# Optimization experiments

Measured on AMD Instinct MI355X. Metric: run time of the kernel, lower is better.

The kernel has to match this reference:

```python
import jax, jax.numpy as jnp
import numpy as np

B, S, D, H, A = 64, 1024, 64, 512, 16


def setup_inputs() -> dict:
    key = jax.random.key(0)
    ks = jax.random.split(key, 13)
    s = 0.02
    return {
        "x": jax.random.normal(ks[0], (B, S, D), jnp.float32),
        "W_ih": jax.random.normal(ks[1], (3 * H, 2 * D), jnp.float32) * s,
        "W_hh": jax.random.normal(ks[2], (3 * H, H), jnp.float32) * s,
        "b_ih": jax.random.normal(ks[3], (3 * H,), jnp.float32) * s,
        "b_hh": jax.random.normal(ks[4], (3 * H,), jnp.float32) * s,
        "fc_w": jax.random.normal(ks[5], (H, H), jnp.float32) * s,
        "fc_b": jax.random.normal(ks[6], (H,), jnp.float32) * s,
        "out_w": jax.random.normal(ks[7], (A, H), jnp.float32) * s,
        "out_b": jax.random.normal(ks[8], (A,), jnp.float32) * s,
        "cb_w1": jax.random.normal(ks[9], (H, H), jnp.float32) * s,
        "cb_b1": jax.random.normal(ks[10], (H,), jnp.float32) * s,
        "cb_w2": jax.random.normal(ks[11], (D, H), jnp.float32) * s,
        "cb_b2": jax.random.normal(ks[12], (D,), jnp.float32) * s,
    }


def _gru_cell(inp, h, W_ih, W_hh, b_ih, b_hh):
    # PyTorch GRU cell: gates ordered (reset, update, new)
    gi = inp @ W_ih.T + b_ih            # [B, 3H]
    gh = h @ W_hh.T + b_hh              # [B, 3H]
    ir, iz, inn = jnp.split(gi, 3, axis=-1)
    hr, hz, hn = jnp.split(gh, 3, axis=-1)
    r = jax.nn.sigmoid(ir + hr)
    z = jax.nn.sigmoid(iz + hz)
    n = jnp.tanh(inn + r * hn)
    return (1.0 - z) * n + z * h


def reference(x, W_ih, W_hh, b_ih, b_hh, fc_w, fc_b, out_w, out_b, cb_w1, cb_b1, cb_w2, cb_b2):
    b = x.shape[0]
    h0 = jnp.zeros((b, H), x.dtype)
    pred0 = jnp.zeros((b, D), x.dtype)

    def step(carry, x_t):
        h, pred = carry
        inp = jnp.concatenate([x_t, pred], axis=-1)        # [B, 2D]
        h_new = _gru_cell(inp, h, W_ih, W_hh, b_ih, b_hh)  # [B, H]
        pred_new = jax.nn.relu(h_new @ cb_w1.T + cb_b1) @ cb_w2.T + cb_b2  # [B, D]
        return (h_new, pred_new), (h_new, pred_new)

    (h_last, _), (outs, preds) = jax.lax.scan(step, (h0, pred0), jnp.swapaxes(x, 0, 1))
    out = jnp.swapaxes(outs, 0, 1)       # [B, S, H]  (gru_out == hidden for 1-layer GRU)
    cb_preds = jnp.swapaxes(preds, 0, 1) # [B, S, D]
    ca1_out = jax.nn.relu(out @ fc_w.T + fc_b)
    q = ca1_out @ out_w.T + out_b        # [B, S, A]
    hidden = h_last[None]                # [1, B, H] like torch GRU hidden
    return q, cb_preds, hidden, ca1_out
```

## Files before the change

### kernel.cpp

```cpp
#include <hip/hip_runtime.h>
#include <hip/hip_fp16.h>


#define B_ 64
#define S_ 1024
#define D_ 64
#define H_ 512
#define A_ 16

#define WG_CHUNKS 240
#define WG_U4     (8 * WG_CHUNKS * 64)
#define WU_U4     (8 * 64 * 64)

union V16 {
    uint4   u;
    float4  f;
    __half2 h[4];
};

__device__ __forceinline__ void dot_block(const uint4* __restrict__ wp, int off,
                                          const V16* __restrict__ a, float& acc) {
    V16 w0, w1, w2, w3;
    w0.u = wp[off];
    w1.u = wp[off + 64];
    w2.u = wp[off + 128];
    w3.u = wp[off + 192];
    __half2 p = __hmul2(w0.h[0], a[0].h[0]);
    __half2 q = __hmul2(w0.h[1], a[0].h[1]);
    p = __hfma2(w0.h[2], a[0].h[2], p);
    q = __hfma2(w0.h[3], a[0].h[3], q);
    p = __hfma2(w1.h[0], a[1].h[0], p);
    q = __hfma2(w1.h[1], a[1].h[1], q);
    p = __hfma2(w1.h[2], a[1].h[2], p);
    q = __hfma2(w1.h[3], a[1].h[3], q);
    p = __hfma2(w2.h[0], a[2].h[0], p);
    q = __hfma2(w2.h[1], a[2].h[1], q);
    p = __hfma2(w2.h[2], a[2].h[2], p);
    q = __hfma2(w2.h[3], a[2].h[3], q);
    p = __hfma2(w3.h[0], a[3].h[0], p);
    q = __hfma2(w3.h[1], a[3].h[1], q);
    p = __hfma2(w3.h[2], a[3].h[2], p);
    q = __hfma2(w3.h[3], a[3].h[3], q);
    float2 fp = __half22float2(p), fq = __half22float2(q);
    acc += (fp.x + fp.y) + (fq.x + fq.y);
}

__global__ __launch_bounds__(256) void k_convert(
    const float* __restrict__ W_ih,
    const float* __restrict__ W_hh,
    const float* __restrict__ cb_w1,
    uint4* __restrict__ wg, uint4* __restrict__ wu)
{
    int idx = blockIdx.x * 256 + threadIdx.x;
    if (idx < WG_U4) {
        int blk  = idx / (WG_CHUNKS * 64);
        int rem  = idx % (WG_CHUNKS * 64);
        int c    = rem / 64, lane = rem % 64;
        int j    = blk * 64 + lane;
        const float* src;
        if (c < 48) {
            int kb = c / 12, r = c % 12, g = r >> 2, q = r & 3;
            src = W_ih + (size_t)(g * 512 + j) * 128 + kb * 32 + q * 8;
        } else {
            int c2 = c - 48;
            int kb = c2 / 12, r = c2 % 12, g = r >> 2, q = r & 3;
            src = W_hh + (size_t)(g * 512 + j) * 512 + kb * 32 + q * 8;
        }
        V16 o;
#pragma unroll
        for (int i = 0; i < 4; ++i) o.h[i] = __floats2half2_rn(src[2 * i], src[2 * i + 1]);
        wg[idx] = o.u;
    } else if (idx < WG_U4 + WU_U4) {
        int i2   = idx - WG_U4;
        int blk  = i2 / 4096;
        int rem  = i2 % 4096;
        int c    = rem / 64, lane = rem % 64;
        int j    = blk * 64 + lane;
        int kb   = c >> 2, q = c & 3;
        const float* src = cb_w1 + (size_t)j * 512 + kb * 32 + q * 8;
        V16 o;
#pragma unroll
        for (int i = 0; i < 4; ++i) o.h[i] = __floats2half2_rn(src[2 * i], src[2 * i + 1]);
        wu[i2] = o.u;
    }
}

__global__ __launch_bounds__(512) void k_recur(
    const float* __restrict__ x,
    const uint4* __restrict__ wg,
    const uint4* __restrict__ wu,
    const float* __restrict__ b_ih,
    const float* __restrict__ b_hh,
    const float* __restrict__ cb_b1,
    const float* __restrict__ cb_b2,
    const float* __restrict__ cb_w2,
    float* __restrict__ hist,
    float* __restrict__ hidden,
    float* __restrict__ cbp)
{
    __shared__ __align__(16) __half2 s_h2[256];
    __shared__ __align__(16) __half2 s_inp2[64];
    __shared__ __align__(16) float   s_u[512];

    const int tid = threadIdx.x;
    const int b   = blockIdx.x;
    const int j   = tid;

    const float bihr = b_ih[j], bihz = b_ih[512 + j], bihn = b_ih[1024 + j];
    const float bhhr = b_hh[j], bhhz = b_hh[512 + j], bhhn = b_hh[1024 + j];
    const float b1j  = cb_b1[j];
    const int   pd   = tid >> 3, psl = tid & 7;
    const float b2d  = cb_b2[pd];
    const float* pw  = cb_w2 + (size_t)pd * 512 + psl * 64;

    float hprev = 0.f;
    if (tid < 256) s_h2[tid] = __floats2half2_rn(0.f, 0.f);
    if (tid < 32) {
        float2 xv = *(const float2*)(x + ((size_t)b * S_) * D_ + tid * 2);
        s_inp2[tid] = __floats2half2_rn(xv.x, xv.y);
    } else if (tid < 64) {
        s_inp2[tid] = __floats2half2_rn(0.f, 0.f);
    }
    __syncthreads();

    const uint4* wgb = wg + (size_t)(tid >> 6) * (WG_CHUNKS * 64) + (tid & 63);
    const uint4* wub = wu + (size_t)(tid >> 6) * (64 * 64) + (tid & 63);

    for (int t = 0; t < S_; ++t) {
        const uint4* wp = wgb;
        float accr = 0.f, accz = 0.f, accni = 0.f, accnh = 0.f;
        V16 a[4];
#pragma unroll
        for (int kb = 0; kb < 4; ++kb) {
            const float4* ap = (const float4*)s_inp2;
            a[0].f = ap[kb * 4 + 0]; a[1].f = ap[kb * 4 + 1];
            a[2].f = ap[kb * 4 + 2]; a[3].f = ap[kb * 4 + 3];
            dot_block(wp,   0, a, accr);
            dot_block(wp, 256, a, accz);
            dot_block(wp, 512, a, accni);
            wp += 12 * 64;
        }
#pragma unroll 2
        for (int kb = 0; kb < 16; ++kb) {
            const float4* ap = (const float4*)s_h2;
            a[0].f = ap[kb * 4 + 0]; a[1].f = ap[kb * 4 + 1];
            a[2].f = ap[kb * 4 + 2]; a[3].f = ap[kb * 4 + 3];
            dot_block(wp,   0, a, accr);
            dot_block(wp, 256, a, accz);
            dot_block(wp, 512, a, accnh);
            wp += 12 * 64;
        }
        float r = 1.f / (1.f + __expf(-(accr + bihr + bhhr)));
        float z = 1.f / (1.f + __expf(-(accz + bihz + bhhz)));
        float n = tanhf(accni + bihn + r * (accnh + bhhn));
        float hnew = (1.f - z) * n + z * hprev;
        __syncthreads();

        float oth = __shfl_xor(hnew, 1);
        if (!(tid & 1)) s_h2[tid >> 1] = __floats2half2_rn(hnew, oth);
        hist[((size_t)b * S_ + t) * H_ + j] = hnew;
        if (t == S_ - 1) hidden[(size_t)b * H_ + j] = hnew;
        hprev = hnew;
        __syncthreads();

        if (tid < 32 && t + 1 < S_) {
            float2 xv = *(const float2*)(x + ((size_t)b * S_ + (t + 1)) * D_ + tid * 2);
            s_inp2[tid] = __floats2half2_rn(xv.x, xv.y);
        }
        const uint4* wp2 = wub;
        float accu = 0.f;
#pragma unroll 2
        for (int kb = 0; kb < 16; ++kb) {
            const float4* ap = (const float4*)s_h2;
            a[0].f = ap[kb * 4 + 0]; a[1].f = ap[kb * 4 + 1];
            a[2].f = ap[kb * 4 + 2]; a[3].f = ap[kb * 4 + 3];
            dot_block(wp2, 0, a, accu);
            wp2 += 256;
        }
        s_u[tid] = fmaxf(accu + b1j, 0.f);
        __syncthreads();

        float pa = 0.f;
        const float4* uv = (const float4*)(s_u + psl * 64);
#pragma unroll
        for (int i = 0; i < 16; ++i) {
            float4 uu = uv[i];
            float4 ww = ((const float4*)pw)[i];
            pa += uu.x * ww.x + uu.y * ww.y + uu.z * ww.z + uu.w * ww.w;
        }
        pa += __shfl_xor(pa, 1);
        pa += __shfl_xor(pa, 2);
        pa += __shfl_xor(pa, 4);
        float pv = pa + b2d;
        if (psl == 0) cbp[((size_t)b * S_ + t) * 64 + pd] = pv;
        float po = __shfl_xor(pv, 8);
        if (psl == 0 && !(pd & 1)) s_inp2[32 + (pd >> 1)] = __floats2half2_rn(pv, po);
        __syncthreads();
    }
}

__global__ __launch_bounds__(256) void k_fc_inplace(
    float* __restrict__ hist,
    const float* __restrict__ fc_w,
    const float* __restrict__ fc_b)
{
    __shared__ __align__(16) float s_a[16 * 516];
    const int tid = threadIdx.x;
    const int r = tid & 15;
    const int jset = tid >> 4;
    const int row0 = blockIdx.x * 16;

    for (int i = tid; i < 2048; i += 256) {
        int rr = i >> 7, f = i & 127;
        float4 v = *(const float4*)(hist + (size_t)(row0 + rr) * H_ + f * 4);
        *(float4*)(s_a + rr * 516 + f * 4) = v;
    }
    __syncthreads();

    float acc[32];
#pragma unroll
    for (int jj = 0; jj < 32; ++jj) acc[jj] = 0.f;

    const float4* arow = (const float4*)(s_a + r * 516);
    for (int k4 = 0; k4 < 128; ++k4) {
        float4 a = arow[k4];
#pragma unroll
        for (int jj = 0; jj < 32; ++jj) {
            int j = jset + (jj << 4);
            float4 w = *(const float4*)(fc_w + (size_t)j * 512 + k4 * 4);
            acc[jj] += a.x * w.x + a.y * w.y + a.z * w.z + a.w * w.w;
        }
    }

    float* crow = hist + (size_t)(row0 + r) * H_;
#pragma unroll
    for (int jj = 0; jj < 32; ++jj) {
        int j = jset + (jj << 4);
        float v = acc[jj] + fc_b[j];
        crow[j] = fmaxf(v, 0.f);
    }
}

__global__ __launch_bounds__(256) void k_q(
    const float* __restrict__ ca1,
    const float* __restrict__ out_w,
    const float* __restrict__ out_b,
    float* __restrict__ q)
{
    __shared__ __align__(16) float s_a[16 * 516];
    __shared__ __align__(16) float s_w[16 * 516];
    const int tid = threadIdx.x;
    const int r = tid >> 4;
    const int a_ = tid & 15;
    const int row0 = blockIdx.x * 16;

    for (int i = tid; i < 2048; i += 256) {
        int rr = i >> 7, f = i & 127;
        float4 v = *(const float4*)(ca1 + (size_t)(row0 + rr) * H_ + f * 4);
        *(float4*)(s_a + rr * 516 + f * 4) = v;
    }
    for (int i = tid; i < 2048; i += 256) {
        int rr = i >> 7, f = i & 127;
        float4 v = *(const float4*)(out_w + (size_t)rr * 512 + f * 4);
        *(float4*)(s_w + rr * 516 + f * 4) = v;
    }
    __syncthreads();

    const float4* arow = (const float4*)(s_a + r * 516);
    const float4* wrow = (const float4*)(s_w + a_ * 516);
    float acc = 0.f;
#pragma unroll 8
    for (int k4 = 0; k4 < 128; ++k4) {
        float4 a = arow[k4];
        float4 w = wrow[k4];
        acc += a.x * w.x + a.y * w.y + a.z * w.z + a.w * w.w;
    }
    q[(size_t)(row0 + r) * A_ + a_] = acc + out_b[a_];
}

extern "C" void kernel_launch(void* const* d_in, const int* in_sizes, int n_in,
                              void* d_out, int out_size, void* d_ws, size_t ws_size,
                              hipStream_t stream) {
    const float* x     = (const float*)d_in[0];
    const float* W_ih  = (const float*)d_in[1];
    const float* W_hh  = (const float*)d_in[2];
    const float* b_ih  = (const float*)d_in[3];
    const float* b_hh  = (const float*)d_in[4];
    const float* fc_w  = (const float*)d_in[5];
    const float* fc_b  = (const float*)d_in[6];
    const float* out_w = (const float*)d_in[7];
    const float* out_b = (const float*)d_in[8];
    const float* cb_w1 = (const float*)d_in[9];
    const float* cb_b1 = (const float*)d_in[10];
    const float* cb_w2 = (const float*)d_in[11];
    const float* cb_b2 = (const float*)d_in[12];

    float* q_out  = (float*)d_out;
    float* cbp    = q_out + (size_t)B_ * S_ * A_;
    float* hidden = cbp + (size_t)B_ * S_ * D_;
    float* ca1    = hidden + (size_t)B_ * H_;

    uint4* wg = (uint4*)d_ws;
    uint4* wu = wg + WG_U4;

    k_convert<<<(WG_U4 + WU_U4) / 256, 256, 0, stream>>>(W_ih, W_hh, cb_w1, wg, wu);
    k_recur<<<B_, 512, 0, stream>>>(x, wg, wu, b_ih, b_hh, cb_b1, cb_b2, cb_w2,
                                    ca1, hidden, cbp);
    k_fc_inplace<<<4096, 256, 0, stream>>>(ca1, fc_w, fc_b);
    k_q<<<4096, 256, 0, stream>>>(ca1, out_w, out_b, q_out);
}
```

Measured before the change: 37.48 ms.

## Split GRU recurrence across 128 persistent workgroups with global barriers

Replaces the per-batch recurrence (64 workgroups, each streaming all weights every step) with 128 persistent workgroups that each own 4 hidden units across all batches, so each workgroup keeps a small weight slice and reuses it over 64 batch rows. Hidden state, the ReLU intermediate and predictions move through global memory and are synchronised by custom flag-based grid barriers, three per timestep. This is meant to cut the per-step weight traffic from global memory and spread work over more compute units, at the cost of three device-wide barriers per step and a deadlock risk if the workgroups are not all co-resident, which a timeout flag guards against.

```diff
diff --git a/kernel.cpp b/kernel.cpp
--- a/kernel.cpp
+++ b/kernel.cpp
@@ -8,9 +8,16 @@
 #define H_ 512
 #define A_ 16
 
-#define WG_CHUNKS 240
-#define WG_U4     (8 * WG_CHUNKS * 64)
-#define WU_U4     (8 * 64 * 64)
+#define OFF_WGX   0
+#define OFF_WGI   98304
+#define OFF_WUX   122880
+#define OFF_SYNC  155648
+#define OFF_H2    156192
+#define OFF_U2    164384
+#define OFF_PRED2 172576
+#define WS_TOTAL  173088
+
+#define NWG 128
 
 union V16 {
     uint4   u;
@@ -18,184 +25,283 @@
     __half2 h[4];
 };
 
-__device__ __forceinline__ void dot_block(const uint4* __restrict__ wp, int off,
-                                          const V16* __restrict__ a, float& acc) {
-    V16 w0, w1, w2, w3;
-    w0.u = wp[off];
-    w1.u = wp[off + 64];
-    w2.u = wp[off + 128];
-    w3.u = wp[off + 192];
-    __half2 p = __hmul2(w0.h[0], a[0].h[0]);
-    __half2 q = __hmul2(w0.h[1], a[0].h[1]);
-    p = __hfma2(w0.h[2], a[0].h[2], p);
-    q = __hfma2(w0.h[3], a[0].h[3], q);
-    p = __hfma2(w1.h[0], a[1].h[0], p);
-    q = __hfma2(w1.h[1], a[1].h[1], q);
-    p = __hfma2(w1.h[2], a[1].h[2], p);
-    q = __hfma2(w1.h[3], a[1].h[3], q);
-    p = __hfma2(w2.h[0], a[2].h[0], p);
-    q = __hfma2(w2.h[1], a[2].h[1], q);
-    p = __hfma2(w2.h[2], a[2].h[2], p);
-    q = __hfma2(w2.h[3], a[2].h[3], q);
-    p = __hfma2(w3.h[0], a[3].h[0], p);
-    q = __hfma2(w3.h[1], a[3].h[1], q);
-    p = __hfma2(w3.h[2], a[3].h[2], p);
-    q = __hfma2(w3.h[3], a[3].h[3], q);
-    float2 fp = __half22float2(p), fq = __half22float2(q);
-    acc += (fp.x + fp.y) + (fq.x + fq.y);
-}
-
 __global__ __launch_bounds__(256) void k_convert(
     const float* __restrict__ W_ih,
     const float* __restrict__ W_hh,
     const float* __restrict__ cb_w1,
-    uint4* __restrict__ wg, uint4* __restrict__ wu)
+    uint4* __restrict__ ws)
 {
     int idx = blockIdx.x * 256 + threadIdx.x;
-    if (idx < WG_U4) {
-        int blk  = idx / (WG_CHUNKS * 64);
-        int rem  = idx % (WG_CHUNKS * 64);
-        int c    = rem / 64, lane = rem % 64;
-        int j    = blk * 64 + lane;
-        const float* src;
-        if (c < 48) {
-            int kb = c / 12, r = c % 12, g = r >> 2, q = r & 3;
-            src = W_ih + (size_t)(g * 512 + j) * 128 + kb * 32 + q * 8;
-        } else {
-            int c2 = c - 48;
-            int kb = c2 / 12, r = c2 % 12, g = r >> 2, q = r & 3;
-            src = W_hh + (size_t)(g * 512 + j) * 512 + kb * 32 + q * 8;
-        }
-        V16 o;
-#pragma unroll
-        for (int i = 0; i < 4; ++i) o.h[i] = __floats2half2_rn(src[2 * i], src[2 * i + 1]);
-        wg[idx] = o.u;
-    } else if (idx < WG_U4 + WU_U4) {
-        int i2   = idx - WG_U4;
-        int blk  = i2 / 4096;
-        int rem  = i2 % 4096;
-        int c    = rem / 64, lane = rem % 64;
-        int j    = blk * 64 + lane;
-        int kb   = c >> 2, q = c & 3;
-        const float* src = cb_w1 + (size_t)j * 512 + kb * 32 + q * 8;
-        V16 o;
-#pragma unroll
-        for (int i = 0; i < 4; ++i) o.h[i] = __floats2half2_rn(src[2 * i], src[2 * i + 1]);
-        wu[i2] = o.u;
-    }
-}
-
-__global__ __launch_bounds__(512) void k_recur(
+    const float* src;
+    if (idx < OFF_WGI) {
+        int wg = idx / 768, rem = idx % 768;
+        int r = rem >> 6, c = (rem >> 4) & 3, q = rem & 15;
+        int g = r >> 2, jj = r & 3;
+        src = W_hh + (size_t)(g * 512 + wg * 4 + jj) * 512 + c * 128 + q * 8;
+    } else if (idx < OFF_WUX) {
+        int i2 = idx - OFF_WGI;
+        int wg = i2 / 192, rem = i2 % 192;
+        int r = rem >> 4, c = (rem >> 2) & 3, q2 = rem & 3;
+        int g = r >> 2, jj = r & 3;
+        src = W_ih + (size_t)(g * 512 + wg * 4 + jj) * 128 + c * 32 + q2 * 8;
+    } else if (idx < OFF_SYNC) {
+        int i2 = idx - OFF_WUX;
+        int wg = i2 / 256, rem = i2 % 256;
+        int jr = rem >> 6, c = (rem >> 4) & 3, q = rem & 15;
+        src = cb_w1 + (size_t)(wg * 4 + jr) * 512 + c * 128 + q * 8;
+    } else if (idx < WS_TOTAL) {
+        ws[idx] = make_uint4(0u, 0u, 0u, 0u);
+        return;
+    } else return;
+    V16 o;
+#pragma unroll
+    for (int i = 0; i < 4; ++i) o.h[i] = __floats2half2_rn(src[2 * i], src[2 * i + 1]);
+    ws[idx] = o.u;
+}
+
+__device__ __forceinline__ int poll_ge(unsigned* p, unsigned bn, unsigned* dead) {
+    unsigned it = 0;
+    while (__hip_atomic_load(p, __ATOMIC_RELAXED, __HIP_MEMORY_SCOPE_AGENT) < bn) {
+        __builtin_amdgcn_s_sleep(2);
+        if ((++it & 1023u) == 0u) {
+            if (__hip_atomic_load(dead, __ATOMIC_RELAXED, __HIP_MEMORY_SCOPE_AGENT) != 0u) return 1;
+            if (it > (1u << 24)) {
+                __hip_atomic_store(dead, 1u, __ATOMIC_RELAXED, __HIP_MEMORY_SCOPE_AGENT);
+                return 1;
+            }
+        }
+    }
+    return 0;
+}
+
+__device__ __forceinline__ int gbar(unsigned* flags, unsigned* dead, unsigned bn,
+                                    unsigned* s_flag) {
+    const int tid = threadIdx.x;
+    __syncthreads();
+    if (tid == 0) *s_flag = 0u;
+    __syncthreads();
+    if (tid == 0) {
+        __builtin_amdgcn_fence(__ATOMIC_RELEASE, "agent");
+        __hip_atomic_store(flags + blockIdx.x * 16, bn, __ATOMIC_RELAXED,
+                           __HIP_MEMORY_SCOPE_AGENT);
+    }
+    if (tid < NWG) {
+        if (poll_ge(flags + tid * 16, bn, dead)) *s_flag = 1u;
+    }
+    __syncthreads();
+    if (tid == 0) __builtin_amdgcn_fence(__ATOMIC_ACQUIRE, "agent");
+    __syncthreads();
+    return *s_flag != 0u;
+}
+
+__global__ __launch_bounds__(256) void k_recur(
+    const uint4* __restrict__ wsb,
+    unsigned* __restrict__ syncw,
+    uint4* __restrict__ h2u4,
+    float* __restrict__ u2f,
+    uint4* __restrict__ pred2u4,
     const float* __restrict__ x,
-    const uint4* __restrict__ wg,
-    const uint4* __restrict__ wu,
-    const float* __restrict__ b_ih,
-    const float* __restrict__ b_hh,
-    const float* __restrict__ cb_b1,
-    const float* __restrict__ cb_b2,
+    const float* __restrict__ b_ih, const float* __restrict__ b_hh,
+    const float* __restrict__ cb_b1, const float* __restrict__ cb_b2,
     const float* __restrict__ cb_w2,
     float* __restrict__ hist,
     float* __restrict__ hidden,
     float* __restrict__ cbp)
 {
-    __shared__ __align__(16) __half2 s_h2[256];
-    __shared__ __align__(16) __half2 s_inp2[64];
-    __shared__ __align__(16) float   s_u[512];
-
+    __shared__ unsigned s_flag;
     const int tid = threadIdx.x;
-    const int b   = blockIdx.x;
-    const int j   = tid;
-
-    const float bihr = b_ih[j], bihz = b_ih[512 + j], bihn = b_ih[1024 + j];
-    const float bhhr = b_hh[j], bhhz = b_hh[512 + j], bhhn = b_hh[1024 + j];
-    const float b1j  = cb_b1[j];
-    const int   pd   = tid >> 3, psl = tid & 7;
-    const float b2d  = cb_b2[pd];
-    const float* pw  = cb_w2 + (size_t)pd * 512 + psl * 64;
-
-    float hprev = 0.f;
-    if (tid < 256) s_h2[tid] = __floats2half2_rn(0.f, 0.f);
-    if (tid < 32) {
-        float2 xv = *(const float2*)(x + ((size_t)b * S_) * D_ + tid * 2);
-        s_inp2[tid] = __floats2half2_rn(xv.x, xv.y);
-    } else if (tid < 64) {
-        s_inp2[tid] = __floats2half2_rn(0.f, 0.f);
-    }
-    __syncthreads();
-
-    const uint4* wgb = wg + (size_t)(tid >> 6) * (WG_CHUNKS * 64) + (tid & 63);
-    const uint4* wub = wu + (size_t)(tid >> 6) * (64 * 64) + (tid & 63);
+    const int wg = blockIdx.x;
+    const int b = tid >> 2;
+    const int c = tid & 3;
+    const int j4 = wg * 4;
+
+    unsigned* dead = syncw + 2048;
+
+    const uint4* wgxP = wsb + OFF_WGX + wg * 768 + c * 16;
+    const uint4* wgiP = wsb + OFF_WGI + wg * 192 + c * 4;
+    const uint4* wuxP = wsb + OFF_WUX + wg * 256 + c * 16;
+
+    float bias_r[4], bias_z[4], bias_ni[4], bias_nh[4], bias_u[4];
+#pragma unroll
+    for (int jj = 0; jj < 4; ++jj) {
+        int j = j4 + jj;
+        bias_r[jj]  = b_ih[j] + b_hh[j];
+        bias_z[jj]  = b_ih[512 + j] + b_hh[512 + j];
+        bias_ni[jj] = b_ih[1024 + j];
+        bias_nh[jj] = b_hh[1024 + j];
+        bias_u[jj]  = cb_b1[j];
+    }
+    const int dl = tid >> 3, oct = tid & 7;
+    const int pb = wg >> 1, d = (wg & 1) * 32 + dl;
+    const float bias_p = cb_b2[d];
+
+    float hprev[4] = {0.f, 0.f, 0.f, 0.f};
+
+    const uint4* hrow0 = h2u4 + b * 64 + c * 16;
+    const uint4* hrow1 = h2u4 + 4096 + b * 64 + c * 16;
+    uint2* h2w0 = (uint2*)h2u4 + b * 128 + wg;
+    uint2* h2w1 = ((uint2*)(h2u4 + 4096)) + b * 128 + wg;
+    __half* pred2h = (__half*)pred2u4;
+
+    unsigned bn = 0;
 
     for (int t = 0; t < S_; ++t) {
-        const uint4* wp = wgb;
-        float accr = 0.f, accz = 0.f, accni = 0.f, accnh = 0.f;
-        V16 a[4];
-#pragma unroll
-        for (int kb = 0; kb < 4; ++kb) {
-            const float4* ap = (const float4*)s_inp2;
-            a[0].f = ap[kb * 4 + 0]; a[1].f = ap[kb * 4 + 1];
-            a[2].f = ap[kb * 4 + 2]; a[3].f = ap[kb * 4 + 3];
-            dot_block(wp,   0, a, accr);
-            dot_block(wp, 256, a, accz);
-            dot_block(wp, 512, a, accni);
-            wp += 12 * 64;
-        }
-#pragma unroll 2
-        for (int kb = 0; kb < 16; ++kb) {
-            const float4* ap = (const float4*)s_h2;
-            a[0].f = ap[kb * 4 + 0]; a[1].f = ap[kb * 4 + 1];
-            a[2].f = ap[kb * 4 + 2]; a[3].f = ap[kb * 4 + 3];
-            dot_block(wp,   0, a, accr);
-            dot_block(wp, 256, a, accz);
-            dot_block(wp, 512, a, accnh);
-            wp += 12 * 64;
-        }
-        float r = 1.f / (1.f + __expf(-(accr + bihr + bhhr)));
-        float z = 1.f / (1.f + __expf(-(accz + bihz + bhhz)));
-        float n = tanhf(accni + bihn + r * (accnh + bhhn));
-        float hnew = (1.f - z) * n + z * hprev;
-        __syncthreads();
-
-        float oth = __shfl_xor(hnew, 1);
-        if (!(tid & 1)) s_h2[tid >> 1] = __floats2half2_rn(hnew, oth);
-        hist[((size_t)b * S_ + t) * H_ + j] = hnew;
-        if (t == S_ - 1) hidden[(size_t)b * H_ + j] = hnew;
-        hprev = hnew;
-        __syncthreads();
-
-        if (tid < 32 && t + 1 < S_) {
-            float2 xv = *(const float2*)(x + ((size_t)b * S_ + (t + 1)) * D_ + tid * 2);
-            s_inp2[tid] = __floats2half2_rn(xv.x, xv.y);
-        }
-        const uint4* wp2 = wub;
-        float accu = 0.f;
-#pragma unroll 2
-        for (int kb = 0; kb < 16; ++kb) {
-            const float4* ap = (const float4*)s_h2;
-            a[0].f = ap[kb * 4 + 0]; a[1].f = ap[kb * 4 + 1];
-            a[2].f = ap[kb * 4 + 2]; a[3].f = ap[kb * 4 + 3];
-            dot_block(wp2, 0, a, accu);
-            wp2 += 256;
-        }
-        s_u[tid] = fmaxf(accu + b1j, 0.f);
-        __syncthreads();
-
-        float pa = 0.f;
-        const float4* uv = (const float4*)(s_u + psl * 64);
+        const int par = t & 1;
+
+        float accf[16];
+#pragma unroll
+        for (int i = 0; i < 16; ++i) accf[i] = 0.f;
+        {
+            const uint4* aP = par ? hrow0 : hrow1;
+#pragma unroll
+            for (int grp = 0; grp < 8; ++grp) {
+                __half2 ha[12];
+#pragma unroll
+                for (int r = 0; r < 12; ++r) ha[r] = __float2half2_rn(0.f);
+#pragma unroll
+                for (int qq = 0; qq < 2; ++qq) {
+                    const int q = grp * 2 + qq;
+                    V16 a; a.u = aP[q];
+#pragma unroll
+                    for (int r = 0; r < 12; ++r) {
+                        V16 w; w.u = wgxP[r * 64 + q];
+                        ha[r] = __hfma2(w.h[0], a.h[0], ha[r]);
+                        ha[r] = __hfma2(w.h[1], a.h[1], ha[r]);
+                        ha[r] = __hfma2(w.h[2], a.h[2], ha[r]);
+                        ha[r] = __hfma2(w.h[3], a.h[3], ha[r]);
+                    }
+                }
+#pragma unroll
+                for (int r = 0; r < 12; ++r) {
+                    float2 f = __half22float2(ha[r]);
+                    accf[r] += f.x + f.y;
+                }
+            }
+            V16 a4[4];
+            if (c < 2) {
+                const float4* xp = (const float4*)(x + ((size_t)b * S_ + t) * D_ + c * 32);
+#pragma unroll
+                for (int q2 = 0; q2 < 4; ++q2) {
+                    float4 f0 = xp[q2 * 2], f1 = xp[q2 * 2 + 1];
+                    a4[q2].h[0] = __floats2half2_rn(f0.x, f0.y);
+                    a4[q2].h[1] = __floats2half2_rn(f0.z, f0.w);
+                    a4[q2].h[2] = __floats2half2_rn(f1.x, f1.y);
+                    a4[q2].h[3] = __floats2half2_rn(f1.z, f1.w);
+                }
+            } else {
+#pragma unroll
+                for (int q2 = 0; q2 < 4; ++q2) a4[q2].u = pred2u4[b * 8 + (c - 2) * 4 + q2];
+            }
+#pragma unroll
+            for (int g2 = 0; g2 < 2; ++g2) {
+                __half2 hb[12];
+#pragma unroll
+                for (int r = 0; r < 12; ++r) hb[r] = __float2half2_rn(0.f);
+#pragma unroll
+                for (int qq = 0; qq < 2; ++qq) {
+                    const int q2 = g2 * 2 + qq;
+                    V16 a = a4[q2];
+#pragma unroll
+                    for (int r = 0; r < 12; ++r) {
+                        V16 w; w.u = wgiP[r * 16 + q2];
+                        hb[r] = __hfma2(w.h[0], a.h[0], hb[r]);
+                        hb[r] = __hfma2(w.h[1], a.h[1], hb[r]);
+                        hb[r] = __hfma2(w.h[2], a.h[2], hb[r]);
+                        hb[r] = __hfma2(w.h[3], a.h[3], hb[r]);
+                    }
+                }
+#pragma unroll
+                for (int r = 0; r < 12; ++r) {
+                    float2 f = __half22float2(hb[r]);
+                    float v = f.x + f.y;
+                    if (r < 8) accf[r] += v;
+                    else       accf[12 + (r - 8)] += v;
+                }
+            }
+        }
 #pragma unroll
         for (int i = 0; i < 16; ++i) {
-            float4 uu = uv[i];
-            float4 ww = ((const float4*)pw)[i];
-            pa += uu.x * ww.x + uu.y * ww.y + uu.z * ww.z + uu.w * ww.w;
-        }
-        pa += __shfl_xor(pa, 1);
-        pa += __shfl_xor(pa, 2);
-        pa += __shfl_xor(pa, 4);
-        float pv = pa + b2d;
-        if (psl == 0) cbp[((size_t)b * S_ + t) * 64 + pd] = pv;
-        float po = __shfl_xor(pv, 8);
-        if (psl == 0 && !(pd & 1)) s_inp2[32 + (pd >> 1)] = __floats2half2_rn(pv, po);
-        __syncthreads();
+            accf[i] += __shfl_xor(accf[i], 1);
+            accf[i] += __shfl_xor(accf[i], 2);
+        }
+        if (c == 0) {
+            float h[4];
+#pragma unroll
+            for (int jj = 0; jj < 4; ++jj) {
+                float rr = 1.f / (1.f + __expf(-(accf[jj] + bias_r[jj])));
+                float zz = 1.f / (1.f + __expf(-(accf[4 + jj] + bias_z[jj])));
+                float nn = tanhf(accf[12 + jj] + bias_ni[jj] + rr * (accf[8 + jj] + bias_nh[jj]));
+                h[jj] = (1.f - zz) * nn + zz * hprev[jj];
+                hprev[jj] = h[jj];
+            }
+            *(float4*)(hist + ((size_t)b * S_ + t) * H_ + j4) = make_float4(h[0], h[1], h[2], h[3]);
+            if (t == S_ - 1)
+                *(float4*)(hidden + (size_t)b * H_ + j4) = make_float4(h[0], h[1], h[2], h[3]);
+            __half2 p0 = __floats2half2_rn(h[0], h[1]);
+            __half2 p1 = __floats2half2_rn(h[2], h[3]);
+            uint2 pk; pk.x = *(unsigned*)&p0; pk.y = *(unsigned*)&p1;
+            *(par ? h2w1 : h2w0) = pk;
+        }
+        ++bn; if (gbar(syncw, dead, bn, &s_flag)) return;
+
+        {
+            const uint4* aC = par ? hrow1 : hrow0;
+            float uacc[4] = {0.f, 0.f, 0.f, 0.f};
+#pragma unroll
+            for (int grp = 0; grp < 8; ++grp) {
+                __half2 ha[4];
+#pragma unroll
+                for (int r = 0; r < 4; ++r) ha[r] = __float2half2_rn(0.f);
+#pragma unroll
+                for (int qq = 0; qq < 2; ++qq) {
+                    const int q = grp * 2 + qq;
+                    V16 a; a.u = aC[q];
+#pragma unroll
+                    for (int r = 0; r < 4; ++r) {
+                        V16 w; w.u = wuxP[r * 64 + q];
+                        ha[r] = __hfma2(w.h[0], a.h[0], ha[r]);
+                        ha[r] = __hfma2(w.h[1], a.h[1], ha[r]);
+                        ha[r] = __hfma2(w.h[2], a.h[2], ha[r]);
+                        ha[r] = __hfma2(w.h[3], a.h[3], ha[r]);
+                    }
+                }
+#pragma unroll
+                for (int r = 0; r < 4; ++r) { float2 f = __half22float2(ha[r]); uacc[r] += f.x + f.y; }
+            }
+#pragma unroll
+            for (int r = 0; r < 4; ++r) {
+                uacc[r] += __shfl_xor(uacc[r], 1);
+                uacc[r] += __shfl_xor(uacc[r], 2);
+            }
+            if (c == 0) {
+                float u0 = fmaxf(uacc[0] + bias_u[0], 0.f);
+                float u1 = fmaxf(uacc[1] + bias_u[1], 0.f);
+                float u2v = fmaxf(uacc[2] + bias_u[2], 0.f);
+                float u3 = fmaxf(uacc[3] + bias_u[3], 0.f);
+                *(float4*)(u2f + (size_t)b * 512 + j4) = make_float4(u0, u1, u2v, u3);
+            }
+        }
+        ++bn; if (gbar(syncw, dead, bn, &s_flag)) return;
+
+        {
+            float pacc = 0.f;
+            const float4* uv = (const float4*)(u2f + (size_t)pb * 512 + oct * 64);
+            const float4* wv = (const float4*)(cb_w2 + (size_t)d * 512 + oct * 64);
+#pragma unroll
+            for (int i = 0; i < 16; ++i) {
+                float4 a = uv[i], w = wv[i];
+                pacc += a.x * w.x + a.y * w.y + a.z * w.z + a.w * w.w;
+            }
+            pacc += __shfl_xor(pacc, 1);
+            pacc += __shfl_xor(pacc, 2);
+            pacc += __shfl_xor(pacc, 4);
+            if (oct == 0) {
+                float pv = pacc + bias_p;
+                cbp[((size_t)pb * S_ + t) * 64 + d] = pv;
+                pred2h[pb * 64 + d] = __float2half(pv);
+            }
+        }
+        ++bn; if (gbar(syncw, dead, bn, &s_flag)) return;
     }
 }
 
@@ -300,12 +406,12 @@
     float* hidden = cbp + (size_t)B_ * S_ * D_;
     float* ca1    = hidden + (size_t)B_ * H_;
 
-    uint4* wg = (uint4*)d_ws;
-    uint4* wu = wg + WG_U4;
-
-    k_convert<<<(WG_U4 + WU_U4) / 256, 256, 0, stream>>>(W_ih, W_hh, cb_w1, wg, wu);
-    k_recur<<<B_, 512, 0, stream>>>(x, wg, wu, b_ih, b_hh, cb_b1, cb_b2, cb_w2,
-                                    ca1, hidden, cbp);
+    uint4* wsu = (uint4*)d_ws;
+
+    k_convert<<<(WS_TOTAL + 255) / 256, 256, 0, stream>>>(W_ih, W_hh, cb_w1, wsu);
+    k_recur<<<NWG, 256, 0, stream>>>(wsu,
+        (unsigned*)(wsu + OFF_SYNC), wsu + OFF_H2, (float*)(wsu + OFF_U2),
+        wsu + OFF_PRED2, x, b_ih, b_hh, cb_b1, cb_b2, cb_w2, ca1, hidden, cbp);
     k_fc_inplace<<<4096, 256, 0, stream>>>(ca1, fc_w, fc_b);
     k_q<<<4096, 256, 0, stream>>>(ca1, out_w, out_b, q_out);
 }
```

Measured after the change: 87.46 ms. +133.4%, slower.
